# Kernel optimization log

Measured on AMD Instinct MI355X. Metric: run time of the kernel, lower is better.

## Reference

```python
import jax, jax.numpy as jnp
import numpy as np

N = 4096
D = 512
H = 3


def setup_inputs() -> dict:
    key = jax.random.key(0)
    k1, k2, k3 = jax.random.split(key, 3)
    graph_info = (jax.random.uniform(k1, (N, N)) < 0.01).astype(jnp.float32)
    h = jax.random.normal(k2, (N, D), dtype=jnp.float32)
    # xavier_normal_ with relu gain: std = sqrt(2) * sqrt(2/(fan_in+fan_out))
    std = np.sqrt(2.0) * np.sqrt(2.0 / (D + H))
    P = jax.random.normal(k3, (D, H), dtype=jnp.float32) * jnp.float32(std)
    return {"graph_info": graph_info, "h": h, "P": P}


def reference(graph_info, h, P):
    # graph_info_1 = spmm(graph_info^T, I)^T == graph_info (identity densification)
    mask = graph_info > 0                                  # [N, N]
    E = jax.nn.relu(h @ P)                                 # [N, H] per-node scores, all heads
    NEG = jnp.float32(-9e15)
    # e is broadcast along rows: att[i, j] = E[j, k] where edge (i->j) exists
    logits = jnp.where(mask[None, :, :], E.T[:, None, :], NEG)  # [H, N, N]
    att = jax.nn.softmax(logits, axis=-1)                  # row-softmax per head
    hh = jnp.einsum('hij,jd->hid', att, h)                 # [H, N, D] aggregate
    # sum_flag == 1: scale each row i by its degree (rowsum of graph_info_1)
    rowsum = jnp.sum(graph_info, axis=-1)                  # [N]
    hh = hh * rowsum[None, :, None]
    # multi_head > 1, concat=False: sum over heads
    return jnp.sum(hh, axis=0)                             # [N, D]
```

## Files before the change

kernel.cpp:

```cpp
#include <hip/hip_runtime.h>
#include <stdint.h>

#define NN 4096
#define DD 512
#define NH 3
#define MAXDEG 256

__device__ __forceinline__ unsigned short f2bf_rn(float x) {
    union { float f; uint32_t u; } v; v.f = x;
    uint32_t u = v.u;
    uint32_t r = (u + 0x7FFFu + ((u >> 16) & 1u)) >> 16;
    return (unsigned short)r;
}
__device__ __forceinline__ float bflo(uint32_t u) {
    union { uint32_t u; float f; } v; v.u = u << 16; return v.f;
}
__device__ __forceinline__ float bfhi(uint32_t u) {
    union { uint32_t u; float f; } v; v.u = u & 0xFFFF0000u; return v.f;
}

__global__ __launch_bounds__(256) void prep_kernel(
    const float* __restrict__ h, const float* __restrict__ P,
    float* __restrict__ w, unsigned short* __restrict__ hb)
{
    int gid = blockIdx.x * 256 + threadIdx.x;
    int row = gid >> 6, ln = gid & 63;
    const float4* h4 = (const float4*)(h + (size_t)row * DD);
    float4 va = h4[ln * 2], vb = h4[ln * 2 + 1];
    float e[8] = { va.x, va.y, va.z, va.w, vb.x, vb.y, vb.z, vb.w };

    uint32_t pk0 = (uint32_t)f2bf_rn(e[0]) | ((uint32_t)f2bf_rn(e[1]) << 16);
    uint32_t pk1 = (uint32_t)f2bf_rn(e[2]) | ((uint32_t)f2bf_rn(e[3]) << 16);
    uint32_t pk2 = (uint32_t)f2bf_rn(e[4]) | ((uint32_t)f2bf_rn(e[5]) << 16);
    uint32_t pk3 = (uint32_t)f2bf_rn(e[6]) | ((uint32_t)f2bf_rn(e[7]) << 16);
    uint4 pk = make_uint4(pk0, pk1, pk2, pk3);
    *(uint4*)(hb + (size_t)row * DD + ln * 8) = pk;

    int d0 = ln * 8;
    float a0 = 0.f, a1 = 0.f, a2 = 0.f;
    #pragma unroll
    for (int k = 0; k < 8; ++k) {
        float hv = e[k];
        const float* Pr = P + (size_t)(d0 + k) * NH;
        a0 = fmaf(hv, Pr[0], a0);
        a1 = fmaf(hv, Pr[1], a1);
        a2 = fmaf(hv, Pr[2], a2);
    }
    #pragma unroll
    for (int off = 32; off > 0; off >>= 1) {
        a0 += __shfl_down(a0, off);
        a1 += __shfl_down(a1, off);
        a2 += __shfl_down(a2, off);
    }
    if (ln == 0) {
        w[row * NH + 0] = expf(fmaxf(a0, 0.f));
        w[row * NH + 1] = expf(fmaxf(a1, 0.f));
        w[row * NH + 2] = expf(fmaxf(a2, 0.f));
    }
}

__global__ __launch_bounds__(256) void att_agg_kernel(
    const float* __restrict__ g, const unsigned short* __restrict__ hb,
    const float* __restrict__ w, float* __restrict__ out)
{
    __shared__ int   s_idx[MAXDEG + 4];
    __shared__ float s_c[MAXDEG + 4];
    __shared__ int   s_cnt;
    __shared__ float s_z[4][3];
    __shared__ float s_part[4][DD];

    const int row = blockIdx.x, tid = threadIdx.x;
    const int wv = tid >> 6, ln = tid & 63;
    if (tid == 0) s_cnt = 0;
    __syncthreads();

    const float4* g4 = (const float4*)(g + (size_t)row * NN);
    #pragma unroll
    for (int it = 0; it < (NN / 4) / 256; ++it) {
        int c4 = it * 256 + tid;
        float4 v = g4[c4];
        float comp[4] = { v.x, v.y, v.z, v.w };
        int base = c4 * 4;
        #pragma unroll
        for (int k = 0; k < 4; ++k) {
            bool p = comp[k] > 0.f;
            unsigned long long m = __ballot(p);
            if (m) {
                int nset = __popcll(m);
                int bpos;
                if (ln == 0) bpos = atomicAdd(&s_cnt, nset);
                bpos = __shfl(bpos, 0);
                if (p) {
                    unsigned pre = __builtin_amdgcn_mbcnt_lo((unsigned)m, 0u);
                    pre = __builtin_amdgcn_mbcnt_hi((unsigned)(m >> 32), pre);
                    int pos = bpos + (int)pre;
                    if (pos < MAXDEG) s_idx[pos] = base + k;
                }
            }
        }
    }
    __syncthreads();
    int nnz = s_cnt; if (nnz > MAXDEG) nnz = MAXDEG;

    if (nnz == 0) {
        ((float2*)(out + (size_t)row * DD))[tid] = make_float2(0.f, 0.f);
        return;
    }

    float z0 = 0.f, z1 = 0.f, z2 = 0.f, w0 = 0.f, w1 = 0.f, w2 = 0.f;
    int myj = 0;
    if (tid < nnz) {
        myj = s_idx[tid];
        const float* wr = w + (size_t)myj * NH;
        w0 = wr[0]; w1 = wr[1]; w2 = wr[2];
        z0 = w0; z1 = w1; z2 = w2;
    }
    #pragma unroll
    for (int off = 32; off > 0; off >>= 1) {
        z0 += __shfl_down(z0, off);
        z1 += __shfl_down(z1, off);
        z2 += __shfl_down(z2, off);
    }
    if (ln == 0) { s_z[wv][0] = z0; s_z[wv][1] = z1; s_z[wv][2] = z2; }
    __syncthreads();
    float Z0 = s_z[0][0] + s_z[1][0] + s_z[2][0] + s_z[3][0];
    float Z1 = s_z[0][1] + s_z[1][1] + s_z[2][1] + s_z[3][1];
    float Z2 = s_z[0][2] + s_z[1][2] + s_z[2][2] + s_z[3][2];
    float RS = (float)nnz;
    float sc0 = RS / Z0, sc1 = RS / Z1, sc2 = RS / Z2;

    int npad = (nnz + 3) & ~3;
    if (tid < nnz) s_c[tid] = fmaf(sc0, w0, fmaf(sc1, w1, sc2 * w2));
    else if (tid < npad) { s_idx[tid] = 0; s_c[tid] = 0.f; }
    __syncthreads();

    int nq = npad >> 2;
    float acc0=0.f,acc1=0.f,acc2=0.f,acc3=0.f,acc4=0.f,acc5=0.f,acc6=0.f,acc7=0.f;
    const unsigned short* hcol = hb + ln * 8;
    int q = 0;
    for (; q + 1 < nq; q += 2) {
        int t0 = q * 4 + wv, t1 = t0 + 4;
        int ja = s_idx[t0]; float ca = s_c[t0];
        int jb = s_idx[t1]; float cb = s_c[t1];
        uint4 ra = *(const uint4*)(hcol + (size_t)ja * DD);
        uint4 rb = *(const uint4*)(hcol + (size_t)jb * DD);
        acc0 = fmaf(ca, bflo(ra.x), acc0); acc1 = fmaf(ca, bfhi(ra.x), acc1);
        acc2 = fmaf(ca, bflo(ra.y), acc2); acc3 = fmaf(ca, bfhi(ra.y), acc3);
        acc4 = fmaf(ca, bflo(ra.z), acc4); acc5 = fmaf(ca, bfhi(ra.z), acc5);
        acc6 = fmaf(ca, bflo(ra.w), acc6); acc7 = fmaf(ca, bfhi(ra.w), acc7);
        acc0 = fmaf(cb, bflo(rb.x), acc0); acc1 = fmaf(cb, bfhi(rb.x), acc1);
        acc2 = fmaf(cb, bflo(rb.y), acc2); acc3 = fmaf(cb, bfhi(rb.y), acc3);
        acc4 = fmaf(cb, bflo(rb.z), acc4); acc5 = fmaf(cb, bfhi(rb.z), acc5);
        acc6 = fmaf(cb, bflo(rb.w), acc6); acc7 = fmaf(cb, bfhi(rb.w), acc7);
    }
    if (q < nq) {
        int t0 = q * 4 + wv;
        int ja = s_idx[t0]; float ca = s_c[t0];
        uint4 ra = *(const uint4*)(hcol + (size_t)ja * DD);
        acc0 = fmaf(ca, bflo(ra.x), acc0); acc1 = fmaf(ca, bfhi(ra.x), acc1);
        acc2 = fmaf(ca, bflo(ra.y), acc2); acc3 = fmaf(ca, bfhi(ra.y), acc3);
        acc4 = fmaf(ca, bflo(ra.z), acc4); acc5 = fmaf(ca, bfhi(ra.z), acc5);
        acc6 = fmaf(ca, bflo(ra.w), acc6); acc7 = fmaf(ca, bfhi(ra.w), acc7);
    }

    float4* sp = (float4*)&s_part[wv][ln * 8];
    sp[0] = make_float4(acc0, acc1, acc2, acc3);
    sp[1] = make_float4(acc4, acc5, acc6, acc7);
    __syncthreads();
    int c0 = tid * 2;
    float2 p0 = *(const float2*)&s_part[0][c0];
    float2 p1 = *(const float2*)&s_part[1][c0];
    float2 p2 = *(const float2*)&s_part[2][c0];
    float2 p3 = *(const float2*)&s_part[3][c0];
    float r0 = (p0.x + p1.x) + (p2.x + p3.x);
    float r1 = (p0.y + p1.y) + (p2.y + p3.y);
    ((float2*)(out + (size_t)row * DD))[tid] = make_float2(r0, r1);
}

extern "C" void kernel_launch(void* const* d_in, const int* in_sizes, int n_in,
                              void* d_out, int out_size, void* d_ws, size_t ws_size,
                              hipStream_t stream) {
    const float* g = (const float*)d_in[0];
    const float* h = (const float*)d_in[1];
    const float* P = (const float*)d_in[2];
    float* out = (float*)d_out;

    float* w = (float*)d_ws;
    unsigned short* hb = (unsigned short*)((char*)d_ws + 65536);

    prep_kernel<<<(NN * 64) / 256, 256, 0, stream>>>(h, P, w, hb);
    att_agg_kernel<<<NN, 256, 0, stream>>>(g, hb, w, out);
}
```

Measured before the change: 113.5 us.

## Split adjacency scan into separate wide kernel writing global neighbor lists

Moves the adjacency-row compaction out of the aggregation kernel into its own kernel with four blocks per row. Each thread issues four ballots and a single global atomic per wave instead of sixteen serialized ballot/atomic steps. The aggregation kernel then reads the count and neighbor list from global memory. The goal is more memory-level parallelism on the 64 MB dense adjacency read, which dominates. The cost is an extra launch, global atomics and a write and read of the neighbor lists. Neighbor order within a row becomes nondeterministic, so float summation order can vary between runs.

```diff
diff --git a/kernel.cpp b/kernel.cpp
--- a/kernel.cpp
+++ b/kernel.cpp
@@ -21,9 +21,11 @@
 
 __global__ __launch_bounds__(256) void prep_kernel(
     const float* __restrict__ h, const float* __restrict__ P,
-    float* __restrict__ w, unsigned short* __restrict__ hb)
+    float* __restrict__ w, unsigned short* __restrict__ hb,
+    int* __restrict__ cnt)
 {
     int gid = blockIdx.x * 256 + threadIdx.x;
+    if (gid < NN) cnt[gid] = 0;
     int row = gid >> 6, ln = gid & 63;
     const float4* h4 = (const float4*)(h + (size_t)row * DD);
     float4 va = h4[ln * 2], vb = h4[ln * 2 + 1];
@@ -33,8 +35,7 @@
     uint32_t pk1 = (uint32_t)f2bf_rn(e[2]) | ((uint32_t)f2bf_rn(e[3]) << 16);
     uint32_t pk2 = (uint32_t)f2bf_rn(e[4]) | ((uint32_t)f2bf_rn(e[5]) << 16);
     uint32_t pk3 = (uint32_t)f2bf_rn(e[6]) | ((uint32_t)f2bf_rn(e[7]) << 16);
-    uint4 pk = make_uint4(pk0, pk1, pk2, pk3);
-    *(uint4*)(hb + (size_t)row * DD + ln * 8) = pk;
+    *(uint4*)(hb + (size_t)row * DD + ln * 8) = make_uint4(pk0, pk1, pk2, pk3);
 
     int d0 = ln * 8;
     float a0 = 0.f, a1 = 0.f, a2 = 0.f;
@@ -59,49 +60,73 @@
     }
 }
 
-__global__ __launch_bounds__(256) void att_agg_kernel(
-    const float* __restrict__ g, const unsigned short* __restrict__ hb,
-    const float* __restrict__ w, float* __restrict__ out)
+__global__ __launch_bounds__(256) void scan_kernel(
+    const float* __restrict__ g, int* __restrict__ cnt,
+    int* __restrict__ rowlist)
+{
+    const int b   = blockIdx.x;
+    const int row = b >> 2;
+    const int seg = b & 3;
+    const int tid = threadIdx.x;
+    const int ln  = tid & 63;
+
+    int c4 = seg * 1024 + tid * 4;
+    float4 v = *(const float4*)(g + (size_t)row * NN + c4);
+
+    bool p0 = v.x > 0.f, p1 = v.y > 0.f, p2 = v.z > 0.f, p3 = v.w > 0.f;
+    unsigned long long m0 = __ballot(p0);
+    unsigned long long m1 = __ballot(p1);
+    unsigned long long m2 = __ballot(p2);
+    unsigned long long m3 = __ballot(p3);
+    int n0 = __popcll(m0), n1 = __popcll(m1), n2 = __popcll(m2), n3 = __popcll(m3);
+    int tot = n0 + n1 + n2 + n3;
+    if (tot == 0) return;
+
+    int base;
+    if (ln == 0) base = atomicAdd(&cnt[row], tot);
+    base = __shfl(base, 0);
+
+    int* rl = rowlist + row * MAXDEG;
+    if (p0) {
+        unsigned pre = __builtin_amdgcn_mbcnt_lo((unsigned)m0, 0u);
+        pre = __builtin_amdgcn_mbcnt_hi((unsigned)(m0 >> 32), pre);
+        int pos = base + (int)pre;
+        if (pos < MAXDEG) rl[pos] = c4 + 0;
+    }
+    if (p1) {
+        unsigned pre = __builtin_amdgcn_mbcnt_lo((unsigned)m1, 0u);
+        pre = __builtin_amdgcn_mbcnt_hi((unsigned)(m1 >> 32), pre);
+        int pos = base + n0 + (int)pre;
+        if (pos < MAXDEG) rl[pos] = c4 + 1;
+    }
+    if (p2) {
+        unsigned pre = __builtin_amdgcn_mbcnt_lo((unsigned)m2, 0u);
+        pre = __builtin_amdgcn_mbcnt_hi((unsigned)(m2 >> 32), pre);
+        int pos = base + n0 + n1 + (int)pre;
+        if (pos < MAXDEG) rl[pos] = c4 + 2;
+    }
+    if (p3) {
+        unsigned pre = __builtin_amdgcn_mbcnt_lo((unsigned)m3, 0u);
+        pre = __builtin_amdgcn_mbcnt_hi((unsigned)(m3 >> 32), pre);
+        int pos = base + n0 + n1 + n2 + (int)pre;
+        if (pos < MAXDEG) rl[pos] = c4 + 3;
+    }
+}
+
+__global__ __launch_bounds__(256) void agg_kernel(
+    const int* __restrict__ cnt, const int* __restrict__ rowlist,
+    const unsigned short* __restrict__ hb, const float* __restrict__ w,
+    float* __restrict__ out)
 {
     __shared__ int   s_idx[MAXDEG + 4];
     __shared__ float s_c[MAXDEG + 4];
-    __shared__ int   s_cnt;
     __shared__ float s_z[4][3];
     __shared__ float s_part[4][DD];
 
     const int row = blockIdx.x, tid = threadIdx.x;
     const int wv = tid >> 6, ln = tid & 63;
-    if (tid == 0) s_cnt = 0;
-    __syncthreads();
-
-    const float4* g4 = (const float4*)(g + (size_t)row * NN);
-    #pragma unroll
-    for (int it = 0; it < (NN / 4) / 256; ++it) {
-        int c4 = it * 256 + tid;
-        float4 v = g4[c4];
-        float comp[4] = { v.x, v.y, v.z, v.w };
-        int base = c4 * 4;
-        #pragma unroll
-        for (int k = 0; k < 4; ++k) {
-            bool p = comp[k] > 0.f;
-            unsigned long long m = __ballot(p);
-            if (m) {
-                int nset = __popcll(m);
-                int bpos;
-                if (ln == 0) bpos = atomicAdd(&s_cnt, nset);
-                bpos = __shfl(bpos, 0);
-                if (p) {
-                    unsigned pre = __builtin_amdgcn_mbcnt_lo((unsigned)m, 0u);
-                    pre = __builtin_amdgcn_mbcnt_hi((unsigned)(m >> 32), pre);
-                    int pos = bpos + (int)pre;
-                    if (pos < MAXDEG) s_idx[pos] = base + k;
-                }
-            }
-        }
-    }
-    __syncthreads();
-    int nnz = s_cnt; if (nnz > MAXDEG) nnz = MAXDEG;
-
+
+    int nnz = cnt[row]; if (nnz > MAXDEG) nnz = MAXDEG;
     if (nnz == 0) {
         ((float2*)(out + (size_t)row * DD))[tid] = make_float2(0.f, 0.f);
         return;
@@ -110,7 +135,7 @@
     float z0 = 0.f, z1 = 0.f, z2 = 0.f, w0 = 0.f, w1 = 0.f, w2 = 0.f;
     int myj = 0;
     if (tid < nnz) {
-        myj = s_idx[tid];
+        myj = rowlist[row * MAXDEG + tid];
         const float* wr = w + (size_t)myj * NH;
         w0 = wr[0]; w1 = wr[1]; w2 = wr[2];
         z0 = w0; z1 = w1; z2 = w2;
@@ -130,7 +155,7 @@
     float sc0 = RS / Z0, sc1 = RS / Z1, sc2 = RS / Z2;
 
     int npad = (nnz + 3) & ~3;
-    if (tid < nnz) s_c[tid] = fmaf(sc0, w0, fmaf(sc1, w1, sc2 * w2));
+    if (tid < nnz) { s_idx[tid] = myj; s_c[tid] = fmaf(sc0, w0, fmaf(sc1, w1, sc2 * w2)); }
     else if (tid < npad) { s_idx[tid] = 0; s_c[tid] = 0.f; }
     __syncthreads();
 
@@ -185,9 +210,12 @@
     const float* P = (const float*)d_in[2];
     float* out = (float*)d_out;
 
-    float* w = (float*)d_ws;
-    unsigned short* hb = (unsigned short*)((char*)d_ws + 65536);
-
-    prep_kernel<<<(NN * 64) / 256, 256, 0, stream>>>(h, P, w, hb);
-    att_agg_kernel<<<NN, 256, 0, stream>>>(g, hb, w, out);
-}
+    float* w            = (float*)d_ws;
+    int* cnt            = (int*)((char*)d_ws + (64 << 10));
+    unsigned short* hb  = (unsigned short*)((char*)d_ws + (128 << 10));
+    int* rowlist        = (int*)((char*)d_ws + (128 << 10) + ((size_t)NN * DD * 2));
+
+    prep_kernel<<<(NN * 64) / 256, 256, 0, stream>>>(h, P, w, hb, cnt);
+    scan_kernel<<<NN * 4, 256, 0, stream>>>(g, cnt, rowlist);
+    agg_kernel<<<NN, 256, 0, stream>>>(cnt, rowlist, hb, w, out);
+}
```

Measured after the change: 135.2 us. 1.19x slower.

## Use per-wave neighbor lists and per-head accumulators to remove block-wide atomics and barriers

Applied to the files above, without the earlier changes.

Each wave now scans its own quarter of the adjacency row and builds a private neighbor list with ballot/mbcnt, with no shared atomic counter. It then aggregates its own neighbors into three per-head accumulators and normalizes by the softmax denominators only at the end. This cuts the number of __syncthreads barriers and drops the separate Z-reduction and coefficient stage. The cost is three times the accumulator registers and shared memory, possible load imbalance between waves, and a per-wave cap of 64 neighbors, which assumes a roughly uniform degree.

```diff
diff --git a/kernel.cpp b/kernel.cpp
--- a/kernel.cpp
+++ b/kernel.cpp
@@ -4,7 +4,7 @@
 #define NN 4096
 #define DD 512
 #define NH 3
-#define MAXDEG 256
+#define WMAX 64
 
 __device__ __forceinline__ unsigned short f2bf_rn(float x) {
     union { float f; uint32_t u; } v; v.f = x;
@@ -33,8 +33,7 @@
     uint32_t pk1 = (uint32_t)f2bf_rn(e[2]) | ((uint32_t)f2bf_rn(e[3]) << 16);
     uint32_t pk2 = (uint32_t)f2bf_rn(e[4]) | ((uint32_t)f2bf_rn(e[5]) << 16);
     uint32_t pk3 = (uint32_t)f2bf_rn(e[6]) | ((uint32_t)f2bf_rn(e[7]) << 16);
-    uint4 pk = make_uint4(pk0, pk1, pk2, pk3);
-    *(uint4*)(hb + (size_t)row * DD + ln * 8) = pk;
+    *(uint4*)(hb + (size_t)row * DD + ln * 8) = make_uint4(pk0, pk1, pk2, pk3);
 
     int d0 = ln * 8;
     float a0 = 0.f, a1 = 0.f, a2 = 0.f;
@@ -63,118 +62,112 @@
     const float* __restrict__ g, const unsigned short* __restrict__ hb,
     const float* __restrict__ w, float* __restrict__ out)
 {
-    __shared__ int   s_idx[MAXDEG + 4];
-    __shared__ float s_c[MAXDEG + 4];
-    __shared__ int   s_cnt;
-    __shared__ float s_z[4][3];
-    __shared__ float s_part[4][DD];
+    __shared__ float s_part[4 * NH * DD];
+    __shared__ int   s_list[4 * WMAX];
+    __shared__ float s_z[4][NH];
+    __shared__ int   s_cw[4];
 
     const int row = blockIdx.x, tid = threadIdx.x;
     const int wv = tid >> 6, ln = tid & 63;
-    if (tid == 0) s_cnt = 0;
-    __syncthreads();
 
-    const float4* g4 = (const float4*)(g + (size_t)row * NN);
+    const float4* g4 = (const float4*)(g + (size_t)row * NN) + wv * 256;
+    float4 v0 = g4[ln], v1 = g4[64 + ln], v2 = g4[128 + ln], v3 = g4[192 + ln];
+
+    int* mylist = s_list + wv * WMAX;
+    int cbase = wv * 1024;
+    int cnt = 0;
+    float4 vs[4] = { v0, v1, v2, v3 };
     #pragma unroll
-    for (int it = 0; it < (NN / 4) / 256; ++it) {
-        int c4 = it * 256 + tid;
-        float4 v = g4[c4];
-        float comp[4] = { v.x, v.y, v.z, v.w };
-        int base = c4 * 4;
+    for (int k = 0; k < 4; ++k) {
+        float comp[4] = { vs[k].x, vs[k].y, vs[k].z, vs[k].w };
+        int col0 = cbase + k * 256 + ln * 4;
         #pragma unroll
-        for (int k = 0; k < 4; ++k) {
-            bool p = comp[k] > 0.f;
+        for (int c = 0; c < 4; ++c) {
+            bool p = comp[c] > 0.f;
             unsigned long long m = __ballot(p);
-            if (m) {
-                int nset = __popcll(m);
-                int bpos;
-                if (ln == 0) bpos = atomicAdd(&s_cnt, nset);
-                bpos = __shfl(bpos, 0);
-                if (p) {
-                    unsigned pre = __builtin_amdgcn_mbcnt_lo((unsigned)m, 0u);
-                    pre = __builtin_amdgcn_mbcnt_hi((unsigned)(m >> 32), pre);
-                    int pos = bpos + (int)pre;
-                    if (pos < MAXDEG) s_idx[pos] = base + k;
-                }
+            if (p) {
+                unsigned pre = __builtin_amdgcn_mbcnt_lo((unsigned)m, 0u);
+                pre = __builtin_amdgcn_mbcnt_hi((unsigned)(m >> 32), pre);
+                int pos = cnt + (int)pre;
+                if (pos < WMAX) mylist[pos] = col0 + c;
+            }
+            cnt += __popcll(m);
+        }
+    }
+    if (cnt > WMAX) cnt = WMAX;
+
+    float accA[8] = {0,0,0,0,0,0,0,0};
+    float accB[8] = {0,0,0,0,0,0,0,0};
+    float accC[8] = {0,0,0,0,0,0,0,0};
+    float z0 = 0.f, z1 = 0.f, z2 = 0.f;
+    const unsigned short* hcol = hb + ln * 8;
+
+    if (cnt > 0) {
+        int j = mylist[0];
+        uint4 rn = *(const uint4*)(hcol + (size_t)j * DD);
+        const float* wr = w + (size_t)j * NH;
+        float wn0 = wr[0], wn1 = wr[1], wn2 = wr[2];
+        for (int t = 0; t < cnt; ++t) {
+            uint4 r = rn;
+            float c0 = wn0, c1 = wn1, c2 = wn2;
+            if (t + 1 < cnt) {
+                int j2 = mylist[t + 1];
+                rn = *(const uint4*)(hcol + (size_t)j2 * DD);
+                const float* wr2 = w + (size_t)j2 * NH;
+                wn0 = wr2[0]; wn1 = wr2[1]; wn2 = wr2[2];
+            }
+            z0 += c0; z1 += c1; z2 += c2;
+            float e[8] = { bflo(r.x), bfhi(r.x), bflo(r.y), bfhi(r.y),
+                           bflo(r.z), bfhi(r.z), bflo(r.w), bfhi(r.w) };
+            #pragma unroll
+            for (int q = 0; q < 8; ++q) {
+                accA[q] = fmaf(c0, e[q], accA[q]);
+                accB[q] = fmaf(c1, e[q], accB[q]);
+                accC[q] = fmaf(c2, e[q], accC[q]);
             }
         }
     }
+
+    {
+        float* base = s_part + (wv * NH + 0) * DD + ln * 8;
+        *(float4*)(base)     = make_float4(accA[0], accA[1], accA[2], accA[3]);
+        *(float4*)(base + 4) = make_float4(accA[4], accA[5], accA[6], accA[7]);
+        base = s_part + (wv * NH + 1) * DD + ln * 8;
+        *(float4*)(base)     = make_float4(accB[0], accB[1], accB[2], accB[3]);
+        *(float4*)(base + 4) = make_float4(accB[4], accB[5], accB[6], accB[7]);
+        base = s_part + (wv * NH + 2) * DD + ln * 8;
+        *(float4*)(base)     = make_float4(accC[0], accC[1], accC[2], accC[3]);
+        *(float4*)(base + 4) = make_float4(accC[4], accC[5], accC[6], accC[7]);
+    }
+    if (ln == 0) { s_z[wv][0] = z0; s_z[wv][1] = z1; s_z[wv][2] = z2; s_cw[wv] = cnt; }
     __syncthreads();
-    int nnz = s_cnt; if (nnz > MAXDEG) nnz = MAXDEG;
 
-    if (nnz == 0) {
-        ((float2*)(out + (size_t)row * DD))[tid] = make_float2(0.f, 0.f);
-        return;
-    }
-
-    float z0 = 0.f, z1 = 0.f, z2 = 0.f, w0 = 0.f, w1 = 0.f, w2 = 0.f;
-    int myj = 0;
-    if (tid < nnz) {
-        myj = s_idx[tid];
-        const float* wr = w + (size_t)myj * NH;
-        w0 = wr[0]; w1 = wr[1]; w2 = wr[2];
-        z0 = w0; z1 = w1; z2 = w2;
-    }
-    #pragma unroll
-    for (int off = 32; off > 0; off >>= 1) {
-        z0 += __shfl_down(z0, off);
-        z1 += __shfl_down(z1, off);
-        z2 += __shfl_down(z2, off);
-    }
-    if (ln == 0) { s_z[wv][0] = z0; s_z[wv][1] = z1; s_z[wv][2] = z2; }
-    __syncthreads();
     float Z0 = s_z[0][0] + s_z[1][0] + s_z[2][0] + s_z[3][0];
     float Z1 = s_z[0][1] + s_z[1][1] + s_z[2][1] + s_z[3][1];
     float Z2 = s_z[0][2] + s_z[1][2] + s_z[2][2] + s_z[3][2];
-    float RS = (float)nnz;
-    float sc0 = RS / Z0, sc1 = RS / Z1, sc2 = RS / Z2;
+    int nnz = s_cw[0] + s_cw[1] + s_cw[2] + s_cw[3];
 
-    int npad = (nnz + 3) & ~3;
-    if (tid < nnz) s_c[tid] = fmaf(sc0, w0, fmaf(sc1, w1, sc2 * w2));
-    else if (tid < npad) { s_idx[tid] = 0; s_c[tid] = 0.f; }
-    __syncthreads();
-
-    int nq = npad >> 2;
-    float acc0=0.f,acc1=0.f,acc2=0.f,acc3=0.f,acc4=0.f,acc5=0.f,acc6=0.f,acc7=0.f;
-    const unsigned short* hcol = hb + ln * 8;
-    int q = 0;
-    for (; q + 1 < nq; q += 2) {
-        int t0 = q * 4 + wv, t1 = t0 + 4;
-        int ja = s_idx[t0]; float ca = s_c[t0];
-        int jb = s_idx[t1]; float cb = s_c[t1];
-        uint4 ra = *(const uint4*)(hcol + (size_t)ja * DD);
-        uint4 rb = *(const uint4*)(hcol + (size_t)jb * DD);
-        acc0 = fmaf(ca, bflo(ra.x), acc0); acc1 = fmaf(ca, bfhi(ra.x), acc1);
-        acc2 = fmaf(ca, bflo(ra.y), acc2); acc3 = fmaf(ca, bfhi(ra.y), acc3);
-        acc4 = fmaf(ca, bflo(ra.z), acc4); acc5 = fmaf(ca, bfhi(ra.z), acc5);
-        acc6 = fmaf(ca, bflo(ra.w), acc6); acc7 = fmaf(ca, bfhi(ra.w), acc7);
-        acc0 = fmaf(cb, bflo(rb.x), acc0); acc1 = fmaf(cb, bfhi(rb.x), acc1);
-        acc2 = fmaf(cb, bflo(rb.y), acc2); acc3 = fmaf(cb, bfhi(rb.y), acc3);
-        acc4 = fmaf(cb, bflo(rb.z), acc4); acc5 = fmaf(cb, bfhi(rb.z), acc5);
-        acc6 = fmaf(cb, bflo(rb.w), acc6); acc7 = fmaf(cb, bfhi(rb.w), acc7);
+    int c0 = tid * 2;
+    float sA0 = 0.f, sA1 = 0.f, sB0 = 0.f, sB1 = 0.f, sC0 = 0.f, sC1 = 0.f;
+    #pragma unroll
+    for (int W = 0; W < 4; ++W) {
+        float2 pa = *(const float2*)(s_part + (W * NH + 0) * DD + c0);
+        float2 pb = *(const float2*)(s_part + (W * NH + 1) * DD + c0);
+        float2 pc = *(const float2*)(s_part + (W * NH + 2) * DD + c0);
+        sA0 += pa.x; sA1 += pa.y;
+        sB0 += pb.x; sB1 += pb.y;
+        sC0 += pc.x; sC1 += pc.y;
     }
-    if (q < nq) {
-        int t0 = q * 4 + wv;
-        int ja = s_idx[t0]; float ca = s_c[t0];
-        uint4 ra = *(const uint4*)(hcol + (size_t)ja * DD);
-        acc0 = fmaf(ca, bflo(ra.x), acc0); acc1 = fmaf(ca, bfhi(ra.x), acc1);
-        acc2 = fmaf(ca, bflo(ra.y), acc2); acc3 = fmaf(ca, bfhi(ra.y), acc3);
-        acc4 = fmaf(ca, bflo(ra.z), acc4); acc5 = fmaf(ca, bfhi(ra.z), acc5);
-        acc6 = fmaf(ca, bflo(ra.w), acc6); acc7 = fmaf(ca, bfhi(ra.w), acc7);
+    float2 res;
+    if (nnz == 0) {
+        res = make_float2(0.f, 0.f);
+    } else {
+        float rs = (float)nnz;
+        float i0 = rs / Z0, i1 = rs / Z1, i2 = rs / Z2;
+        res.x = fmaf(sA0, i0, fmaf(sB0, i1, sC0 * i2));
+        res.y = fmaf(sA1, i0, fmaf(sB1, i1, sC1 * i2));
     }
-
-    float4* sp = (float4*)&s_part[wv][ln * 8];
-    sp[0] = make_float4(acc0, acc1, acc2, acc3);
-    sp[1] = make_float4(acc4, acc5, acc6, acc7);
-    __syncthreads();
-    int c0 = tid * 2;
-    float2 p0 = *(const float2*)&s_part[0][c0];
-    float2 p1 = *(const float2*)&s_part[1][c0];
-    float2 p2 = *(const float2*)&s_part[2][c0];
-    float2 p3 = *(const float2*)&s_part[3][c0];
-    float r0 = (p0.x + p1.x) + (p2.x + p3.x);
-    float r1 = (p0.y + p1.y) + (p2.y + p3.y);
-    ((float2*)(out + (size_t)row * DD))[tid] = make_float2(r0, r1);
+    ((float2*)(out + (size_t)row * DD))[tid] = res;
 }
 
 extern "C" void kernel_launch(void* const* d_in, const int* in_sizes, int n_in,
@@ -185,8 +178,8 @@
     const float* P = (const float*)d_in[2];
     float* out = (float*)d_out;
 
-    float* w = (float*)d_ws;
-    unsigned short* hb = (unsigned short*)((char*)d_ws + 65536);
+    float* w           = (float*)d_ws;
+    unsigned short* hb = (unsigned short*)((char*)d_ws + (64 << 10));
 
     prep_kernel<<<(NN * 64) / 256, 256, 0, stream>>>(h, P, w, hb);
     att_agg_kernel<<<NN, 256, 0, stream>>>(g, hb, w, out);
```

Result: slower. 118.0 us (+4.0%).
